# Kernel tuning notes

Measured on AMD Instinct MI355X. Metric: run time of the kernel, lower is better.

## Reference

```python
import jax, jax.numpy as jnp
import numpy as np

B, K, D, NH = 4096, 32, 1024, 16
HD = D // NH
LN_EPS = 1e-5
RMS_EPS = 1e-6


def layernorm(x, g, b):
    mu = jnp.mean(x, axis=-1, keepdims=True)
    var = jnp.mean((x - mu) ** 2, axis=-1, keepdims=True)
    return (x - mu) * jax.lax.rsqrt(var + LN_EPS) * g + b


def rmsnorm(x, g):
    ms = jnp.mean(x ** 2, axis=-1, keepdims=True)
    return x * jax.lax.rsqrt(ms + RMS_EPS) * g


def setup_inputs() -> dict:
    key = jax.random.key(0)
    ks = jax.random.split(key, 12)
    s = 0.02
    inp = {
        "query": jax.random.normal(ks[0], (B, D), jnp.float32),
        "point_features": jax.random.normal(ks[1], (B, K, D), jnp.float32),
        "lnq_g": jnp.ones((D,), jnp.float32),
        "lnq_b": jnp.zeros((D,), jnp.float32),
        "lnkv_g": jnp.ones((D,), jnp.float32),
        "lnkv_b": jnp.zeros((D,), jnp.float32),
        "Wq": jax.random.normal(ks[2], (D, D), jnp.float32) * s,
        "bq": jnp.zeros((D,), jnp.float32),
        "Wk": jax.random.normal(ks[3], (D, D), jnp.float32) * s,
        "bk": jnp.zeros((D,), jnp.float32),
        "Wv": jax.random.normal(ks[4], (D, D), jnp.float32) * s,
        "bv": jnp.zeros((D,), jnp.float32),
        "rmsq_g": jnp.ones((D,), jnp.float32),
        "rmsk_g": jnp.ones((D,), jnp.float32),
        "Wo": jax.random.normal(ks[5], (D, D), jnp.float32) * s,
        "bo": jnp.zeros((D,), jnp.float32),
        "mlpn_g": jnp.ones((D,), jnp.float32),
        "mlpn_b": jnp.zeros((D,), jnp.float32),
        "W1": jax.random.normal(ks[6], (D, 4 * D), jnp.float32) * s,
        "b1": jnp.zeros((4 * D,), jnp.float32),
        "W2": jax.random.normal(ks[7], (4 * D, D), jnp.float32) * s,
        "b2": jnp.zeros((D,), jnp.float32),
    }
    return inp


def reference(query, point_features, lnq_g, lnq_b, lnkv_g, lnkv_b,
              Wq, bq, Wk, bk, Wv, bv, rmsq_g, rmsk_g, Wo, bo,
              mlpn_g, mlpn_b, W1, b1, W2, b2):
    q_in = layernorm(query, lnq_g, lnq_b)            # [B, D]
    kv_in = layernorm(point_features, lnkv_g, lnkv_b)  # [B, K, D]

    q = rmsnorm(q_in @ Wq + bq, rmsq_g)              # [B, D]
    k = rmsnorm(kv_in @ Wk + bk, rmsk_g)             # [B, K, D]
    v = kv_in @ Wv + bv                               # [B, K, D]

    # Faithful to original: raw row-major reshape [B,K,D] -> [B,NH,K,HD]
    qh = q.reshape(B, NH, HD)                         # [B, NH, HD] (q_len = 1)
    kh = k.reshape(B, NH, K, HD)
    vh = v.reshape(B, NH, K, HD)

    scores = jnp.einsum('bhd,bhkd->bhk', qh, kh) / np.sqrt(HD).astype(np.float32)
    attn = jax.nn.softmax(scores, axis=-1)            # [B, NH, K]
    out = jnp.einsum('bhk,bhkd->bhd', attn, vh)       # [B, NH, HD]

    # Faithful: transpose(1,2) then reshape -> [B, HD, NH] -> [B, D]
    out = jnp.transpose(out, (0, 2, 1)).reshape(B, D)
    out = (out @ Wo + bo) + query                     # residual

    h = layernorm(out, mlpn_g, mlpn_b)
    mlp_out = (jax.nn.gelu(h @ W1 + b1, approximate=False) @ W2) + b2
    return out + mlp_out
```

## Files before the change

### kernel.cpp

```cpp
#include <hip/hip_runtime.h>
#include <stdint.h>

#define DEVI __device__ __forceinline__

typedef unsigned short u16;
typedef short s8v __attribute__((ext_vector_type(8)));
typedef float f4v __attribute__((ext_vector_type(4)));
typedef u16 u16x4 __attribute__((ext_vector_type(4)));

DEVI u16 f2bf(float f) {
  unsigned u = __float_as_uint(f);
  u += 0x7fffu + ((u >> 16) & 1u);
  return (u16)(u >> 16);
}
DEVI float bf2f(u16 h) { return __uint_as_float(((unsigned)h) << 16); }

DEVI void gload16(const void* g, void* l) {
  __builtin_amdgcn_global_load_lds(
      (const __attribute__((address_space(1))) void*)(uintptr_t)g,
      (__attribute__((address_space(3))) void*)(uintptr_t)l, 16, 0, 0);
}

__global__ __launch_bounds__(256) void transpose_w(const float* __restrict__ W,
                                                   u16* __restrict__ Wt, int R, int C) {
  __shared__ float tile[32][33];
  const int tx = threadIdx.x & 31, ty = threadIdx.x >> 5;
  const int r0 = blockIdx.y * 32, c0 = blockIdx.x * 32;
#pragma unroll
  for (int i = 0; i < 4; ++i)
    tile[ty + 8 * i][tx] = W[(size_t)(r0 + ty + 8 * i) * C + c0 + tx];
  __syncthreads();
#pragma unroll
  for (int i = 0; i < 4; ++i)
    Wt[(size_t)(c0 + ty + 8 * i) * R + r0 + tx] = f2bf(tile[tx][ty + 8 * i]);
}

__global__ __launch_bounds__(256) void ln_rows(const float* __restrict__ x,
                                               const float* __restrict__ g,
                                               const float* __restrict__ bsh,
                                               u16* __restrict__ y,
                                               float* __restrict__ zbuf) {
  const size_t row = blockIdx.x;
  const int t = threadIdx.x;
  if (zbuf && t == 0) zbuf[row] = 0.f;
  float4 v = ((const float4*)(x + row * 1024))[t];
  float s = v.x + v.y + v.z + v.w;
  float q = v.x * v.x + v.y * v.y + v.z * v.z + v.w * v.w;
#pragma unroll
  for (int m = 1; m < 64; m <<= 1) { s += __shfl_xor(s, m); q += __shfl_xor(q, m); }
  __shared__ float sh[8];
  if ((t & 63) == 0) { sh[t >> 6] = s; sh[4 + (t >> 6)] = q; }
  __syncthreads();
  s = sh[0] + sh[1] + sh[2] + sh[3];
  q = sh[4] + sh[5] + sh[6] + sh[7];
  const float mu = s * (1.f / 1024.f);
  const float var = q * (1.f / 1024.f) - mu * mu;
  const float rs = rsqrtf(var + 1e-5f);
  const int c = t * 4;
  const float in[4] = {v.x, v.y, v.z, v.w};
  u16x4 o;
#pragma unroll
  for (int i = 0; i < 4; ++i) o[i] = f2bf((in[i] - mu) * rs * g[c + i] + bsh[c + i]);
  *(u16x4*)(y + row * 1024 + c) = o;
}

template <int EPI, int KK>
__global__ __launch_bounds__(512, 2) void gemm256(
    const u16* __restrict__ A, const u16* __restrict__ Bt,
    const float* __restrict__ biasK, const float* __restrict__ biasV,
    const float* __restrict__ gcol, u16* __restrict__ CK, u16* __restrict__ CV,
    float* __restrict__ rowssq, int M, int N, int RB, int CB) {
  __shared__ u16 lds[4][16384];
  const int t = threadIdx.x;
  const int lane = t & 63;
  const int wave = t >> 6;
  const int wm = wave >> 2, wn = wave & 3;
  const int fr = lane & 15, kq = lane >> 4;

  const int bid = blockIdx.x;
  const int cpx = gridDim.x >> 3;
  const int swz = (bid & 7) * cpx + (bid >> 3);
  const int rb = swz / CB, cb = swz % CB;
  const size_t row0 = (size_t)rb * 256, col0 = (size_t)cb * 256;

  f4v acc[8][4];
#pragma unroll
  for (int i = 0; i < 8; ++i)
#pragma unroll
    for (int n = 0; n < 4; ++n) acc[i][n] = (f4v){0.f, 0.f, 0.f, 0.f};

  const int srow = t >> 2;
  const int scol = (((t & 3) ^ ((t >> 3) & 3)) << 3);
  const u16* Ag0 = A + (row0 + srow) * (size_t)KK + scol;
  const u16* Ag1 = Ag0 + (size_t)128 * KK;
  const u16* Bg0 = Bt + (col0 + srow) * (size_t)KK + scol;
  const u16* Bg1 = Bg0 + (size_t)128 * KK;

  const int kxb = ((kq ^ ((fr >> 1) & 3)) << 4);
  const char* lbase = (const char*)&lds[0][0];
  const char* bA[4];
  const char* bB[4];
  char* dst0[4];
#pragma unroll
  for (int s = 0; s < 4; ++s) {
    bA[s] = lbase + s * 32768 + wm * 8192 + fr * 64 + kxb;
    bB[s] = lbase + s * 32768 + 16384 + wn * 4096 + fr * 64 + kxb;
    dst0[s] = (char*)lbase + s * 32768 + t * 16;
  }

#pragma unroll
  for (int tt = 0; tt < 3; ++tt) {
    gload16(Ag0 + tt * 32, dst0[tt]);
    gload16(Ag1 + tt * 32, dst0[tt] + 8192);
    gload16(Bg0 + tt * 32, dst0[tt] + 16384);
    gload16(Bg1 + tt * 32, dst0[tt] + 24576);
  }

  s8v aX[8], aY[8], b[4];
  asm volatile("s_waitcnt vmcnt(8)" ::: "memory");
  __builtin_amdgcn_s_barrier();
  __builtin_amdgcn_sched_barrier(0);
#pragma unroll
  for (int m = 0; m < 4; ++m) {
    aX[m] = *(const s8v*)(bA[0] + m * 1024);
    aX[4 + m] = *(const s8v*)(bA[0] + 4096 + m * 1024);
  }

#define GEMM_ITER(T_, CUR, NXT)                                                  \
  {                                                                              \
    asm volatile("s_waitcnt vmcnt(4)" ::: "memory");                             \
    __builtin_amdgcn_s_barrier();                                                \
    __builtin_amdgcn_sched_barrier(0);                                           \
    {                             \
      char* d = dst0[(T_ + 3) & 3];                                              \
      gload16(Ag0 + (T_ + 3) * 32, d);                                           \
      gload16(Ag1 + (T_ + 3) * 32, d + 8192);                                    \
      gload16(Bg0 + (T_ + 3) * 32, d + 16384);                                   \
      gload16(Bg1 + (T_ + 3) * 32, d + 24576);                                   \
    }                                                                            \
    _Pragma("unroll") for (int n = 0; n < 4; ++n)                                \
        b[n] = *(const s8v*)(bB[T_ & 3] + n * 1024);                             \
    _Pragma("unroll") for (int m = 0; m < 4; ++m) {                              \
      NXT[m] = *(const s8v*)(bA[(T_ + 1) & 3] + m * 1024);                       \
      NXT[4 + m] = *(const s8v*)(bA[(T_ + 1) & 3] + 4096 + m * 1024);            \
    }                                                                            \
    __builtin_amdgcn_s_setprio(1);                                               \
    _Pragma("unroll") for (int m = 0; m < 4; ++m)                                \
        _Pragma("unroll") for (int n = 0; n < 4; ++n)                            \
            acc[m][n] =                                                          \
        __builtin_amdgcn_mfma_f32_16x16x32_bf16(CUR[m], b[n], acc[m][n], 0, 0, 0); \
    _Pragma("unroll") for (int m = 0; m < 4; ++m)                                \
        _Pragma("unroll") for (int n = 0; n < 4; ++n)                            \
            acc[4 + m][n] = __builtin_amdgcn_mfma_f32_16x16x32_bf16(             \
                CUR[4 + m], b[n], acc[4 + m][n], 0, 0, 0);                       \
    __builtin_amdgcn_s_setprio(0);                                               \
  }

  const int NT = KK >> 5;
#pragma unroll 2
  for (int T = 0; T < NT; T += 2) {
    GEMM_ITER(T, aX, aY);
    GEMM_ITER((T + 1), aY, aX);
  }
#undef GEMM_ITER

  const int kq4 = kq * 4;
  if (EPI == 0) {
    const bool isK = (col0 < 1024);
    if (isK) {
#pragma unroll
      for (int ai = 0; ai < 8; ++ai) {
        int cols[4];
        float bb[4], gg[4];
#pragma unroll
        for (int n = 0; n < 4; ++n) {
          cols[n] = (int)col0 + wn * 64 + n * 16 + fr;
          bb[n] = biasK[cols[n]];
          gg[n] = gcol[cols[n]];
        }
#pragma unroll
        for (int r = 0; r < 4; ++r) {
          const size_t grow = row0 + wm * 128 + ai * 16 + kq4 + r;
          float v[4];
#pragma unroll
          for (int n = 0; n < 4; ++n) v[n] = acc[ai][n][r] + bb[n];
          float s = v[0] * v[0] + v[1] * v[1] + v[2] * v[2] + v[3] * v[3];
          s += __shfl_xor(s, 1);
          s += __shfl_xor(s, 2);
          s += __shfl_xor(s, 4);
          s += __shfl_xor(s, 8);
          if (fr == 0) atomicAdd(&rowssq[grow], s);
#pragma unroll
          for (int n = 0; n < 4; ++n)
            CK[grow * 1024 + cols[n]] = f2bf(v[n] * gg[n]);
        }
      }
    } else {
#pragma unroll
      for (int ai = 0; ai < 8; ++ai) {
        int cols[4];
        float bb[4];
#pragma unroll
        for (int n = 0; n < 4; ++n) {
          cols[n] = (int)col0 - 1024 + wn * 64 + n * 16 + fr;
          bb[n] = biasV[cols[n]];
        }
#pragma unroll
        for (int r = 0; r < 4; ++r) {
          const size_t grow = row0 + wm * 128 + ai * 16 + kq4 + r;
#pragma unroll
          for (int n = 0; n < 4; ++n)
            CV[grow * 1024 + cols[n]] = f2bf(acc[ai][n][r] + bb[n]);
        }
      }
    }
  } else {
#pragma unroll
    for (int ai = 0; ai < 8; ++ai) {
      int cols[4];
      float bb[4];
#pragma unroll
      for (int n = 0; n < 4; ++n) {
        cols[n] = (int)col0 + wn * 64 + n * 16 + fr;
        bb[n] = biasK[cols[n]];
      }
#pragma unroll
      for (int r = 0; r < 4; ++r) {
        const size_t grow = row0 + wm * 128 + ai * 16 + kq4 + r;
#pragma unroll
        for (int n = 0; n < 4; ++n) {
          const float x = acc[ai][n][r] + bb[n];
          CK[grow * (size_t)N + cols[n]] = f2bf(0.5f * x * (1.f + erff(x * 0.70710678118654752f)));
        }
      }
    }
  }
}

template <int EPI>
__global__ __launch_bounds__(256) void gemm_bt(
    const u16* __restrict__ A, const u16* __restrict__ Bt,
    const float* __restrict__ bias, const float* __restrict__ gcol,
    void* __restrict__ Cv, const float* __restrict__ extra,
    float* __restrict__ rowssq, int M, int N, int K) {
  __shared__ u16 As[128 * 32];
  __shared__ u16 Bs[128 * 32];
  const int t = threadIdx.x;
  const int lane = t & 63;
  const int wave = t >> 6;
  const int wr = wave >> 1, wc = wave & 1;
  const size_t row0 = (size_t)blockIdx.y * 128;
  const size_t col0 = (size_t)blockIdx.x * 128;
  int Ksub = K, koff = 0;
  if (EPI == 6) { Ksub = K / gridDim.z; koff = blockIdx.z * Ksub; }

  f4v acc[4][4];
#pragma unroll
  for (int m = 0; m < 4; ++m)
#pragma unroll
    for (int n = 0; n < 4; ++n) acc[m][n] = (f4v){0.f, 0.f, 0.f, 0.f};

  const int sr = t >> 2;
  const int scw = (((t & 3) ^ ((t >> 3) & 3)) << 3);
  const u16* Ag = A + (row0 + sr) * (size_t)K + koff + scw;
  const u16* Bg = Bt + (col0 + sr) * (size_t)K + koff + scw;
  u16* Al = &As[t * 8];
  u16* Bl = &Bs[t * 8];
  const int fr = lane & 15;
  const int kx = (((lane >> 4) ^ ((fr >> 1) & 3)) << 3);

  for (int k0 = 0; k0 < Ksub; k0 += 32) {
    gload16(Ag + k0, Al);
    gload16(Ag + k0 + (size_t)64 * K, Al + 64 * 32);
    gload16(Bg + k0, Bl);
    gload16(Bg + k0 + (size_t)64 * K, Bl + 64 * 32);
    __syncthreads();
    s8v a[4], b[4];
#pragma unroll
    for (int m = 0; m < 4; ++m)
      a[m] = *(const s8v*)&As[(wr * 64 + m * 16 + fr) * 32 + kx];
#pragma unroll
    for (int n = 0; n < 4; ++n)
      b[n] = *(const s8v*)&Bs[(wc * 64 + n * 16 + fr) * 32 + kx];
#pragma unroll
    for (int m = 0; m < 4; ++m)
#pragma unroll
      for (int n = 0; n < 4; ++n)
        acc[m][n] = __builtin_amdgcn_mfma_f32_16x16x32_bf16(a[m], b[n], acc[m][n], 0, 0, 0);
    __syncthreads();
  }

  float* Cp = (float*)Cv;
  if (EPI == 6) Cp += (size_t)blockIdx.z * M * (size_t)N;
  const int rg = (lane >> 4) * 4;
#pragma unroll
  for (int m = 0; m < 4; ++m) {
    int cols[4];
    float bvals[4];
#pragma unroll
    for (int n = 0; n < 4; ++n) {
      cols[n] = (int)col0 + wc * 64 + n * 16 + fr;
      bvals[n] = (EPI == 6) ? 0.f : bias[cols[n]];
    }
#pragma unroll
    for (int r = 0; r < 4; ++r) {
      const size_t grow = row0 + wr * 64 + m * 16 + rg + r;
      float v[4];
#pragma unroll
      for (int n = 0; n < 4; ++n) v[n] = acc[m][n][r] + bvals[n];
      if (EPI == 5) {
        float s = v[0] * v[0] + v[1] * v[1] + v[2] * v[2] + v[3] * v[3];
        s += __shfl_xor(s, 1);
        s += __shfl_xor(s, 2);
        s += __shfl_xor(s, 4);
        s += __shfl_xor(s, 8);
        if (fr == 0) atomicAdd(&rowssq[grow], s);
      }
#pragma unroll
      for (int n = 0; n < 4; ++n) {
        const size_t idx = grow * (size_t)N + cols[n];
        if (EPI == 3) {
          Cp[idx] = v[n] + extra[idx];
        } else if (EPI == 5) {
          ((u16*)Cv)[idx] = f2bf(v[n]);
        } else if (EPI == 6) {
          Cp[idx] = v[n];
        }
      }
    }
  }
}

__global__ __launch_bounds__(256) void attn_k(const u16* __restrict__ qf,
                                              const u16* __restrict__ kmat,
                                              const float* __restrict__ kssq,
                                              const u16* __restrict__ vmat,
                                              const float* __restrict__ gq,
                                              const float* __restrict__ qssq,
                                              u16* __restrict__ ao) {
  const int lb = blockIdx.x;
  const int t = threadIdx.x;
  const int wave = t >> 6, lane = t & 63;
  const int j = lane & 31, half = lane >> 5;
  const float rq = rsqrtf(qssq[lb] * (1.f / 1024.f) + 1e-6f) * 0.125f;
  __shared__ float po[64][17];
#pragma unroll
  for (int hi = 0; hi < 4; ++hi) {
    const int h = wave * 4 + hi;
    const int krow = lb * 32 + 2 * h + (j >> 4);
    const u16* kp = kmat + (size_t)krow * 1024 + (j & 15) * 64 + half * 32;
    const u16* qp = qf + (size_t)lb * 1024 + h * 64 + half * 32;
    const float* gqp = gq + h * 64 + half * 32;
    float s = 0.f;
#pragma unroll
    for (int cc = 0; cc < 4; ++cc) {
      s8v qv = *(const s8v*)(qp + cc * 8);
      s8v kv = *(const s8v*)(kp + cc * 8);
#pragma unroll
      for (int e = 0; e < 8; ++e)
        s += bf2f((u16)qv[e]) * gqp[cc * 8 + e] * bf2f((u16)kv[e]);
    }
    s += __shfl_xor(s, 32);
    s *= rsqrtf(kssq[krow] * (1.f / 1024.f) + 1e-6f) * rq;
    float mx = s;
#pragma unroll
    for (int m = 16; m >= 1; m >>= 1) mx = fmaxf(mx, __shfl_xor(mx, m));
    const float pe = __expf(s - mx);
    float sum = pe;
#pragma unroll
    for (int m = 16; m >= 1; m >>= 1) sum += __shfl_xor(sum, m);
    const float pr = pe / sum;
    float o = 0.f;
#pragma unroll
    for (int jj = 0; jj < 32; ++jj) {
      const int vrow = lb * 32 + 2 * h + (jj >> 4);
      const float vv = bf2f(vmat[(size_t)vrow * 1024 + (jj & 15) * 64 + lane]);
      o += __shfl(pr, jj) * vv;
    }
    po[lane][h] = o;
  }
  __syncthreads();
  const int c = t * 4;
  u16x4 o4;
#pragma unroll
  for (int i = 0; i < 4; ++i) o4[i] = f2bf(po[(c + i) >> 4][(c + i) & 15]);
  *(u16x4*)(ao + (size_t)lb * 1024 + c) = o4;
}

__global__ __launch_bounds__(256) void combine_k(const float* __restrict__ p0,
                                                 const float* __restrict__ p1,
                                                 const float* __restrict__ b2,
                                                 const float* __restrict__ resid,
                                                 float* __restrict__ out) {
  const int i = blockIdx.x * 256 + threadIdx.x;
  float4 a = ((const float4*)p0)[i];
  float4 b = ((const float4*)p1)[i];
  float4 r = ((const float4*)resid)[i];
  float4 bb = ((const float4*)b2)[i & 255];
  float4 o;
  o.x = a.x + b.x + r.x + bb.x;
  o.y = a.y + b.y + r.y + bb.y;
  o.z = a.z + b.z + r.z + bb.z;
  o.w = a.w + b.w + r.w + bb.w;
  ((float4*)out)[i] = o;
}

extern "C" void kernel_launch(void* const* d_in, const int* in_sizes, int n_in,
                              void* d_out, int out_size, void* d_ws, size_t ws_size,
                              hipStream_t stream) {
  const float* query  = (const float*)d_in[0];
  const float* pf     = (const float*)d_in[1];
  const float* lnq_g  = (const float*)d_in[2];
  const float* lnq_b  = (const float*)d_in[3];
  const float* lnkv_g = (const float*)d_in[4];
  const float* lnkv_b = (const float*)d_in[5];
  const float* Wq     = (const float*)d_in[6];
  const float* bq     = (const float*)d_in[7];
  const float* Wk     = (const float*)d_in[8];
  const float* bk     = (const float*)d_in[9];
  const float* Wv     = (const float*)d_in[10];
  const float* bv     = (const float*)d_in[11];
  const float* rmsq_g = (const float*)d_in[12];
  const float* rmsk_g = (const float*)d_in[13];
  const float* Wo     = (const float*)d_in[14];
  const float* bo     = (const float*)d_in[15];
  const float* mlpn_g = (const float*)d_in[16];
  const float* mlpn_b = (const float*)d_in[17];
  const float* W1     = (const float*)d_in[18];
  const float* b1     = (const float*)d_in[19];
  const float* W2     = (const float*)d_in[20];
  const float* b2     = (const float*)d_in[21];
  float* out = (float*)d_out;

  char* p = (char*)d_ws;
  auto alloc = [&](size_t n) {
    char* r = p;
    p += (n + 255) & ~(size_t)255;
    return r;
  };

  u16* Wqt = (u16*)alloc((size_t)1024 * 1024 * 2);
  u16* KVt = (u16*)alloc((size_t)2048 * 1024 * 2);
  u16* Wot = (u16*)alloc((size_t)1024 * 1024 * 2);
  u16* W1t = (u16*)alloc((size_t)1024 * 4096 * 2);
  u16* W2t = (u16*)alloc((size_t)4096 * 1024 * 2);
  u16* qln = (u16*)alloc((size_t)4096 * 1024 * 2);
  u16* qpre = (u16*)alloc((size_t)4096 * 1024 * 2);
  float* qssq = (float*)alloc((size_t)4096 * 4);
  u16* attn_o = (u16*)alloc((size_t)4096 * 1024 * 2);
  float* outbuf = (float*)alloc((size_t)4096 * 1024 * 4);
  u16* hbuf = (u16*)alloc((size_t)4096 * 1024 * 2);
  u16* mid = (u16*)alloc((size_t)4096 * 4096 * 2);
  float* w2p = (float*)alloc((size_t)2 * 4096 * 1024 * 4);

  const size_t used = (size_t)(p - (char*)d_ws);
  int NC = 4;
  while (NC < 64) {
    size_t rows_try = (size_t)131072 / NC;
    if (used + 3 * (rows_try * 2048 + 256) + rows_try * 4 + 256 <= ws_size) break;
    NC *= 2;
  }
  const size_t rows = (size_t)131072 / NC;
  u16* kvln = (u16*)alloc(rows * 2048);
  u16* kmat = (u16*)alloc(rows * 2048);
  u16* vmat = (u16*)alloc(rows * 2048);
  float* kssq = (float*)alloc(rows * 4);

  transpose_w<<<dim3(32, 32), 256, 0, stream>>>(Wq, Wqt, 1024, 1024);
  transpose_w<<<dim3(32, 32), 256, 0, stream>>>(Wk, KVt, 1024, 1024);
  transpose_w<<<dim3(32, 32), 256, 0, stream>>>(Wv, KVt + (size_t)1024 * 1024, 1024, 1024);
  transpose_w<<<dim3(32, 32), 256, 0, stream>>>(Wo, Wot, 1024, 1024);
  transpose_w<<<dim3(128, 32), 256, 0, stream>>>(W1, W1t, 1024, 4096);
  transpose_w<<<dim3(32, 128), 256, 0, stream>>>(W2, W2t, 4096, 1024);

  ln_rows<<<4096, 256, 0, stream>>>(query, lnq_g, lnq_b, qln, qssq);
  gemm_bt<5><<<dim3(8, 32), 256, 0, stream>>>(qln, Wqt, bq, nullptr, qpre, nullptr,
                                              qssq, 4096, 1024, 1024);

  const int bpc = 4096 / NC;
  const int RB = (int)(rows / 256);
  for (int c = 0; c < NC; ++c) {
    ln_rows<<<(unsigned)rows, 256, 0, stream>>>(pf + (size_t)c * rows * 1024, lnkv_g,
                                                lnkv_b, kvln, kssq);
    gemm256<0, 1024><<<RB * 8, 512, 0, stream>>>(kvln, KVt, bk, bv, rmsk_g, kmat, vmat,
                                                 kssq, (int)rows, 2048, RB, 8);
    attn_k<<<bpc, 256, 0, stream>>>(qpre + (size_t)c * bpc * 1024, kmat, kssq, vmat,
                                    rmsq_g, qssq + (size_t)c * bpc,
                                    attn_o + (size_t)c * bpc * 1024);
  }

  gemm_bt<3><<<dim3(8, 32), 256, 0, stream>>>(attn_o, Wot, bo, nullptr, outbuf, query,
                                              nullptr, 4096, 1024, 1024);
  ln_rows<<<4096, 256, 0, stream>>>(outbuf, mlpn_g, mlpn_b, hbuf, nullptr);
  gemm256<1, 1024><<<16 * 16, 512, 0, stream>>>(hbuf, W1t, b1, nullptr, nullptr, mid,
                                                nullptr, nullptr, 4096, 4096, 16, 16);
  gemm_bt<6><<<dim3(8, 32, 2), 256, 0, stream>>>(mid, W2t, nullptr, nullptr, w2p,
                                                 nullptr, nullptr, 4096, 1024, 4096);
  combine_k<<<4096, 256, 0, stream>>>(w2p, w2p + (size_t)4096 * 1024, b2, outbuf, out);
}
```

Before: 1.062 ms.

## Restructure GEMM main loop to double-buffered BK=64 tiles with interleaved loads

Replaces the 4-stage BK=32 LDS ring with a 2-stage BK=64 double buffer. Each K-step splits the MFMA work into four quadrants and interleaves the next tile's global-to-LDS loads and the LDS fragment reads between them, with one barrier per 64-wide step instead of one per 32. The LDS row swizzle is changed to match the 128-byte rows. The intent is to halve barrier count and overlap memory with compute better, at the cost of shallower prefetch depth and a full vmcnt(0) wait every step.

```diff
diff --git a/kernel.cpp b/kernel.cpp
--- a/kernel.cpp
+++ b/kernel.cpp
@@ -70,7 +70,7 @@
     const float* __restrict__ biasK, const float* __restrict__ biasV,
     const float* __restrict__ gcol, u16* __restrict__ CK, u16* __restrict__ CV,
     float* __restrict__ rowssq, int M, int N, int RB, int CB) {
-  __shared__ u16 lds[4][16384];
+  __shared__ u16 lds[2][32768];
   const int t = threadIdx.x;
   const int lane = t & 63;
   const int wave = t >> 6;
@@ -89,80 +89,123 @@
 #pragma unroll
     for (int n = 0; n < 4; ++n) acc[i][n] = (f4v){0.f, 0.f, 0.f, 0.f};
 
-  const int srow = t >> 2;
-  const int scol = (((t & 3) ^ ((t >> 3) & 3)) << 3);
-  const u16* Ag0 = A + (row0 + srow) * (size_t)KK + scol;
-  const u16* Ag1 = Ag0 + (size_t)128 * KK;
-  const u16* Bg0 = Bt + (col0 + srow) * (size_t)KK + scol;
-  const u16* Bg1 = Bg0 + (size_t)128 * KK;
-
-  const int kxb = ((kq ^ ((fr >> 1) & 3)) << 4);
-  const char* lbase = (const char*)&lds[0][0];
-  const char* bA[4];
-  const char* bB[4];
-  char* dst0[4];
-#pragma unroll
-  for (int s = 0; s < 4; ++s) {
-    bA[s] = lbase + s * 32768 + wm * 8192 + fr * 64 + kxb;
-    bB[s] = lbase + s * 32768 + 16384 + wn * 4096 + fr * 64 + kxb;
-    dst0[s] = (char*)lbase + s * 32768 + t * 16;
-  }
-
-#pragma unroll
-  for (int tt = 0; tt < 3; ++tt) {
-    gload16(Ag0 + tt * 32, dst0[tt]);
-    gload16(Ag1 + tt * 32, dst0[tt] + 8192);
-    gload16(Bg0 + tt * 32, dst0[tt] + 16384);
-    gload16(Bg1 + tt * 32, dst0[tt] + 24576);
-  }
-
-  s8v aX[8], aY[8], b[4];
-  asm volatile("s_waitcnt vmcnt(8)" ::: "memory");
+  const int srow = t >> 3;
+  const int scol = (((t & 7) ^ (srow & 7)) << 3);
+  const u16* Ag = A + (row0 + srow) * (size_t)KK + scol;
+  const u16* Bg = Bt + (col0 + srow) * (size_t)KK + scol;
+  char* dA[2];
+  char* dB[2];
+  const char* lb = (const char*)&lds[0][0];
+#pragma unroll
+  for (int s = 0; s < 2; ++s) {
+    dA[s] = (char*)lb + s * 65536 + t * 16;
+    dB[s] = (char*)lb + s * 65536 + 32768 + t * 16;
+  }
+
+  const int f7 = fr & 7;
+  const int kx0 = ((kq ^ f7) << 4);
+  const int kx1 = kx0 ^ 64;
+  const char* bA[2][2];
+  const char* bB[2][2];
+#pragma unroll
+  for (int s = 0; s < 2; ++s) {
+    bA[s][0] = lb + s * 65536 + (wm * 128 + fr) * 128 + kx0;
+    bA[s][1] = lb + s * 65536 + (wm * 128 + fr) * 128 + kx1;
+    bB[s][0] = lb + s * 65536 + 32768 + (wn * 64 + fr) * 128 + kx0;
+    bB[s][1] = lb + s * 65536 + 32768 + (wn * 64 + fr) * 128 + kx1;
+  }
+
+  const int NT = KK >> 6;
+
+#pragma unroll
+  for (int j = 0; j < 4; ++j) {
+    gload16(Ag + (size_t)j * 64 * KK, dA[0] + j * 8192);
+    gload16(Bg + (size_t)j * 64 * KK, dB[0] + j * 8192);
+  }
+  asm volatile("s_waitcnt vmcnt(0)" ::: "memory");
   __builtin_amdgcn_s_barrier();
   __builtin_amdgcn_sched_barrier(0);
-#pragma unroll
-  for (int m = 0; m < 4; ++m) {
-    aX[m] = *(const s8v*)(bA[0] + m * 1024);
-    aX[4 + m] = *(const s8v*)(bA[0] + 4096 + m * 1024);
-  }
-
-#define GEMM_ITER(T_, CUR, NXT)                                                  \
+
+#define KV_ITER(T_, SL, SN)                                                      \
   {                                                                              \
-    asm volatile("s_waitcnt vmcnt(4)" ::: "memory");                             \
+    const int Ts = (T_ + 1 < NT) ? T_ + 1 : NT - 1;                              \
+    const u16* Agt = Ag + (size_t)Ts * 64;                                       \
+    const u16* Bgt = Bg + (size_t)Ts * 64;                                       \
+    s8v a[8], b0[4], b1[4];                                                      \
+                                          \
+    _Pragma("unroll") for (int m = 0; m < 4; ++m) {                              \
+      a[2 * m] = *(const s8v*)(bA[SL][0] + m * 2048);                            \
+      a[2 * m + 1] = *(const s8v*)(bA[SL][1] + m * 2048);                        \
+    }                                                                            \
+    _Pragma("unroll") for (int n = 0; n < 2; ++n) {                              \
+      b0[2 * n] = *(const s8v*)(bB[SL][0] + n * 2048);                           \
+      b0[2 * n + 1] = *(const s8v*)(bB[SL][1] + n * 2048);                       \
+    }                                                                            \
+    gload16(Agt, dA[SN]);                                                        \
+    gload16(Agt + (size_t)64 * KK, dA[SN] + 8192);                               \
+    __builtin_amdgcn_s_setprio(1);                                               \
+    _Pragma("unroll") for (int m = 0; m < 4; ++m)                                \
+        _Pragma("unroll") for (int n = 0; n < 2; ++n) {                          \
+      acc[m][n] = __builtin_amdgcn_mfma_f32_16x16x32_bf16(a[2 * m], b0[2 * n],   \
+                                                          acc[m][n], 0, 0, 0);   \
+      acc[m][n] = __builtin_amdgcn_mfma_f32_16x16x32_bf16(                       \
+          a[2 * m + 1], b0[2 * n + 1], acc[m][n], 0, 0, 0);                      \
+    }                                                                            \
+    __builtin_amdgcn_s_setprio(0);                                               \
+                                          \
+    _Pragma("unroll") for (int n = 0; n < 2; ++n) {                              \
+      b1[2 * n] = *(const s8v*)(bB[SL][0] + 4096 + n * 2048);                    \
+      b1[2 * n + 1] = *(const s8v*)(bB[SL][1] + 4096 + n * 2048);                \
+    }                                                                            \
+    gload16(Agt + (size_t)128 * KK, dA[SN] + 16384);                             \
+    gload16(Agt + (size_t)192 * KK, dA[SN] + 24576);                             \
+    __builtin_amdgcn_s_setprio(1);                                               \
+    _Pragma("unroll") for (int m = 0; m < 4; ++m)                                \
+        _Pragma("unroll") for (int n = 0; n < 2; ++n) {                          \
+      acc[m][2 + n] = __builtin_amdgcn_mfma_f32_16x16x32_bf16(                   \
+          a[2 * m], b1[2 * n], acc[m][2 + n], 0, 0, 0);                          \
+      acc[m][2 + n] = __builtin_amdgcn_mfma_f32_16x16x32_bf16(                   \
+          a[2 * m + 1], b1[2 * n + 1], acc[m][2 + n], 0, 0, 0);                  \
+    }                                                                            \
+    __builtin_amdgcn_s_setprio(0);                                               \
+                             \
+    _Pragma("unroll") for (int m = 0; m < 4; ++m) {                              \
+      a[2 * m] = *(const s8v*)(bA[SL][0] + 8192 + m * 2048);                     \
+      a[2 * m + 1] = *(const s8v*)(bA[SL][1] + 8192 + m * 2048);                 \
+    }                                                                            \
+    gload16(Bgt, dB[SN]);                                                        \
+    gload16(Bgt + (size_t)64 * KK, dB[SN] + 8192);                               \
+    __builtin_amdgcn_s_setprio(1);                                               \
+    _Pragma("unroll") for (int m = 0; m < 4; ++m)                                \
+        _Pragma("unroll") for (int n = 0; n < 2; ++n) {                          \
+      acc[4 + m][2 + n] = __builtin_amdgcn_mfma_f32_16x16x32_bf16(               \
+          a[2 * m], b1[2 * n], acc[4 + m][2 + n], 0, 0, 0);                      \
+      acc[4 + m][2 + n] = __builtin_amdgcn_mfma_f32_16x16x32_bf16(               \
+          a[2 * m + 1], b1[2 * n + 1], acc[4 + m][2 + n], 0, 0, 0);              \
+    }                                                                            \
+    __builtin_amdgcn_s_setprio(0);                                               \
+                           \
+    gload16(Bgt + (size_t)128 * KK, dB[SN] + 16384);                             \
+    gload16(Bgt + (size_t)192 * KK, dB[SN] + 24576);                             \
+    __builtin_amdgcn_s_setprio(1);                                               \
+    _Pragma("unroll") for (int m = 0; m < 4; ++m)                                \
+        _Pragma("unroll") for (int n = 0; n < 2; ++n) {                          \
+      acc[4 + m][n] = __builtin_amdgcn_mfma_f32_16x16x32_bf16(                   \
+          a[2 * m], b0[2 * n], acc[4 + m][n], 0, 0, 0);                          \
+      acc[4 + m][n] = __builtin_amdgcn_mfma_f32_16x16x32_bf16(                   \
+          a[2 * m + 1], b0[2 * n + 1], acc[4 + m][n], 0, 0, 0);                  \
+    }                                                                            \
+    __builtin_amdgcn_s_setprio(0);                                               \
+    asm volatile("s_waitcnt vmcnt(0)" ::: "memory");                             \
     __builtin_amdgcn_s_barrier();                                                \
     __builtin_amdgcn_sched_barrier(0);                                           \
-    {                             \
-      char* d = dst0[(T_ + 3) & 3];                                              \
-      gload16(Ag0 + (T_ + 3) * 32, d);                                           \
-      gload16(Ag1 + (T_ + 3) * 32, d + 8192);                                    \
-      gload16(Bg0 + (T_ + 3) * 32, d + 16384);                                   \
-      gload16(Bg1 + (T_ + 3) * 32, d + 24576);                                   \
-    }                                                                            \
-    _Pragma("unroll") for (int n = 0; n < 4; ++n)                                \
-        b[n] = *(const s8v*)(bB[T_ & 3] + n * 1024);                             \
-    _Pragma("unroll") for (int m = 0; m < 4; ++m) {                              \
-      NXT[m] = *(const s8v*)(bA[(T_ + 1) & 3] + m * 1024);                       \
-      NXT[4 + m] = *(const s8v*)(bA[(T_ + 1) & 3] + 4096 + m * 1024);            \
-    }                                                                            \
-    __builtin_amdgcn_s_setprio(1);                                               \
-    _Pragma("unroll") for (int m = 0; m < 4; ++m)                                \
-        _Pragma("unroll") for (int n = 0; n < 4; ++n)                            \
-            acc[m][n] =                                                          \
-        __builtin_amdgcn_mfma_f32_16x16x32_bf16(CUR[m], b[n], acc[m][n], 0, 0, 0); \
-    _Pragma("unroll") for (int m = 0; m < 4; ++m)                                \
-        _Pragma("unroll") for (int n = 0; n < 4; ++n)                            \
-            acc[4 + m][n] = __builtin_amdgcn_mfma_f32_16x16x32_bf16(             \
-                CUR[4 + m], b[n], acc[4 + m][n], 0, 0, 0);                       \
-    __builtin_amdgcn_s_setprio(0);                                               \
-  }
-
-  const int NT = KK >> 5;
-#pragma unroll 2
+  }
+
   for (int T = 0; T < NT; T += 2) {
-    GEMM_ITER(T, aX, aY);
-    GEMM_ITER((T + 1), aY, aX);
-  }
-#undef GEMM_ITER
+    KV_ITER(T, 0, 1);
+    KV_ITER((T + 1), 1, 0);
+  }
+#undef KV_ITER
 
   const int kq4 = kq * 4;
   if (EPI == 0) {
```

Result: faster. 1.035 ms (median of 2 runs) (-2.6%).

## Replace 4-stage LDS pipeline with 2-stage double buffering in gemm256

Applied to the files above, without the earlier changes.

Cuts the GEMM's shared-memory staging from four buffers to two, halving LDS use per block. Global-to-LDS prefetch now runs only one tile ahead, with two barriers per iteration. The A-fragment register double buffering (aX/aY) is also removed, so each iteration loads its A fragments from LDS right before its MFMAs. This reduces LDS footprint and register pressure, possibly letting more blocks fit per CU. The cost is shallower latency hiding, more barriers, and a redundant clamped load on the last iteration.

```diff
diff --git a/kernel.cpp b/kernel.cpp
--- a/kernel.cpp
+++ b/kernel.cpp
@@ -70,7 +70,7 @@
     const float* __restrict__ biasK, const float* __restrict__ biasV,
     const float* __restrict__ gcol, u16* __restrict__ CK, u16* __restrict__ CV,
     float* __restrict__ rowssq, int M, int N, int RB, int CB) {
-  __shared__ u16 lds[4][16384];
+  __shared__ u16 lds[2][16384];
   const int t = threadIdx.x;
   const int lane = t & 63;
   const int wave = t >> 6;
@@ -91,78 +91,63 @@
 
   const int srow = t >> 2;
   const int scol = (((t & 3) ^ ((t >> 3) & 3)) << 3);
-  const u16* Ag0 = A + (row0 + srow) * (size_t)KK + scol;
-  const u16* Ag1 = Ag0 + (size_t)128 * KK;
-  const u16* Bg0 = Bt + (col0 + srow) * (size_t)KK + scol;
-  const u16* Bg1 = Bg0 + (size_t)128 * KK;
+  const u16* Ag = A + (row0 + srow) * (size_t)KK + scol;
+  const u16* Bg = Bt + (col0 + srow) * (size_t)KK + scol;
+  char* dA[2];
+  char* dB[2];
+  const char* lb = (const char*)&lds[0][0];
+#pragma unroll
+  for (int s = 0; s < 2; ++s) {
+    dA[s] = (char*)lb + s * 32768 + t * 16;
+    dB[s] = (char*)lb + s * 32768 + 16384 + t * 16;
+  }
 
   const int kxb = ((kq ^ ((fr >> 1) & 3)) << 4);
-  const char* lbase = (const char*)&lds[0][0];
-  const char* bA[4];
-  const char* bB[4];
-  char* dst0[4];
-#pragma unroll
-  for (int s = 0; s < 4; ++s) {
-    bA[s] = lbase + s * 32768 + wm * 8192 + fr * 64 + kxb;
-    bB[s] = lbase + s * 32768 + 16384 + wn * 4096 + fr * 64 + kxb;
-    dst0[s] = (char*)lbase + s * 32768 + t * 16;
-  }
-
-#pragma unroll
-  for (int tt = 0; tt < 3; ++tt) {
-    gload16(Ag0 + tt * 32, dst0[tt]);
-    gload16(Ag1 + tt * 32, dst0[tt] + 8192);
-    gload16(Bg0 + tt * 32, dst0[tt] + 16384);
-    gload16(Bg1 + tt * 32, dst0[tt] + 24576);
-  }
-
-  s8v aX[8], aY[8], b[4];
-  asm volatile("s_waitcnt vmcnt(8)" ::: "memory");
-  __builtin_amdgcn_s_barrier();
-  __builtin_amdgcn_sched_barrier(0);
-#pragma unroll
-  for (int m = 0; m < 4; ++m) {
-    aX[m] = *(const s8v*)(bA[0] + m * 1024);
-    aX[4 + m] = *(const s8v*)(bA[0] + 4096 + m * 1024);
-  }
-
-#define GEMM_ITER(T_, CUR, NXT)                                                  \
+  const char* bA[2];
+  const char* bB[2];
+#pragma unroll
+  for (int s = 0; s < 2; ++s) {
+    bA[s] = lb + s * 32768 + (wm * 128 + fr) * 64 + kxb;
+    bB[s] = lb + s * 32768 + 16384 + (wn * 64 + fr) * 64 + kxb;
+  }
+
+  const int NT = KK >> 5;
+
+  gload16(Ag, dA[0]);
+  gload16(Ag + (size_t)128 * KK, dA[0] + 8192);
+  gload16(Bg, dB[0]);
+  gload16(Bg + (size_t)128 * KK, dB[0] + 8192);
+
+#define KV_ITER(T_, SL, SN)                                                      \
   {                                                                              \
-    asm volatile("s_waitcnt vmcnt(4)" ::: "memory");                             \
-    __builtin_amdgcn_s_barrier();                                                \
-    __builtin_amdgcn_sched_barrier(0);                                           \
-    {                             \
-      char* d = dst0[(T_ + 3) & 3];                                              \
-      gload16(Ag0 + (T_ + 3) * 32, d);                                           \
-      gload16(Ag1 + (T_ + 3) * 32, d + 8192);                                    \
-      gload16(Bg0 + (T_ + 3) * 32, d + 16384);                                   \
-      gload16(Bg1 + (T_ + 3) * 32, d + 24576);                                   \
-    }                                                                            \
+    __builtin_amdgcn_s_barrier();           \
+    const int Ts = (T_ + 1 < NT) ? T_ + 1 : NT - 1;                              \
+    const u16* Agt = Ag + (size_t)Ts * 32;                                       \
+    const u16* Bgt = Bg + (size_t)Ts * 32;                                       \
+    gload16(Agt, dA[SN]);                                                        \
+    gload16(Agt + (size_t)128 * KK, dA[SN] + 8192);                              \
+    gload16(Bgt, dB[SN]);                                                        \
+    gload16(Bgt + (size_t)128 * KK, dB[SN] + 8192);                              \
+    asm volatile("s_waitcnt vmcnt(4)" ::: "memory");          \
+    __builtin_amdgcn_s_barrier();                      \
+    s8v a[8], b[4];                                                              \
+    _Pragma("unroll") for (int i = 0; i < 8; ++i)                                \
+        a[i] = *(const s8v*)(bA[SL] + i * 1024);                                 \
     _Pragma("unroll") for (int n = 0; n < 4; ++n)                                \
-        b[n] = *(const s8v*)(bB[T_ & 3] + n * 1024);                             \
-    _Pragma("unroll") for (int m = 0; m < 4; ++m) {                              \
-      NXT[m] = *(const s8v*)(bA[(T_ + 1) & 3] + m * 1024);                       \
-      NXT[4 + m] = *(const s8v*)(bA[(T_ + 1) & 3] + 4096 + m * 1024);            \
-    }                                                                            \
+        b[n] = *(const s8v*)(bB[SL] + n * 1024);                                 \
     __builtin_amdgcn_s_setprio(1);                                               \
-    _Pragma("unroll") for (int m = 0; m < 4; ++m)                                \
+    _Pragma("unroll") for (int i = 0; i < 8; ++i)                                \
         _Pragma("unroll") for (int n = 0; n < 4; ++n)                            \
-            acc[m][n] =                                                          \
-        __builtin_amdgcn_mfma_f32_16x16x32_bf16(CUR[m], b[n], acc[m][n], 0, 0, 0); \
-    _Pragma("unroll") for (int m = 0; m < 4; ++m)                                \
-        _Pragma("unroll") for (int n = 0; n < 4; ++n)                            \
-            acc[4 + m][n] = __builtin_amdgcn_mfma_f32_16x16x32_bf16(             \
-                CUR[4 + m], b[n], acc[4 + m][n], 0, 0, 0);                       \
+            acc[i][n] =                                                          \
+        __builtin_amdgcn_mfma_f32_16x16x32_bf16(a[i], b[n], acc[i][n], 0, 0, 0); \
     __builtin_amdgcn_s_setprio(0);                                               \
   }
 
-  const int NT = KK >> 5;
-#pragma unroll 2
   for (int T = 0; T < NT; T += 2) {
-    GEMM_ITER(T, aX, aY);
-    GEMM_ITER((T + 1), aY, aX);
-  }
-#undef GEMM_ITER
+    KV_ITER(T, 0, 1);
+    KV_ITER((T + 1), 1, 0);
+  }
+#undef KV_ITER
 
   const int kq4 = kq * 4;
   if (EPI == 0) {
```

After: 1.077 ms. About the same (+1.4%).
